# Kernel optimization log

Hardware: AMD Instinct MI355X
Metric: run time of the kernel (lower is better)

Reference implementation:

```python
import jax, jax.numpy as jnp
import numpy as np

H = 768            # hidden_size
IMG_H = 1024       # image_hidden_size
NH = 12            # num_heads
NKV = 1            # num_kv_heads (MQA)
HD = H // NH       # head_dim = 64
FF = 4 * H         # intermediate_size = 3072
EPS = 1e-5


def layernorm(x, g, b):
    m = jnp.mean(x, axis=-1, keepdims=True)
    v = jnp.mean(jnp.square(x - m), axis=-1, keepdims=True)
    return (x - m) * jax.lax.rsqrt(v + EPS) * g + b


def setup_inputs() -> dict:
    key = jax.random.key(0)
    ks = jax.random.split(key, 12)
    B, NQ, NIMG = 8, 256, 4096
    s = 0.02
    return {
        "hidden_states": jax.random.normal(ks[0], (B, NQ, H), jnp.float32),
        "image_features": jax.random.normal(ks[1], (B, NIMG, IMG_H), jnp.float32),
        # norm_image_pre
        "ln_img_g": jnp.ones((IMG_H,), jnp.float32),
        "ln_img_b": jnp.zeros((IMG_H,), jnp.float32),
        # image_bottleneck (bias=False)
        "W_bottle": jax.random.normal(ks[2], (IMG_H, H), jnp.float32) * s,
        # norm_hidden
        "ln_h_g": jnp.ones((H,), jnp.float32),
        "ln_h_b": jnp.zeros((H,), jnp.float32),
        # to_q
        "Wq": jax.random.normal(ks[3], (H, H), jnp.float32) * s,
        "bq": jnp.zeros((H,), jnp.float32),
        # to_kv: out = num_kv_heads * head_dim * 2
        "Wkv": jax.random.normal(ks[4], (H, 2 * NKV * HD), jnp.float32) * s,
        "bkv": jnp.zeros((2 * NKV * HD,), jnp.float32),
        # to_out
        "Wo": jax.random.normal(ks[5], (H, H), jnp.float32) * s,
        "bo": jnp.zeros((H,), jnp.float32),
        # attn_out_norm
        "ln_ao_g": jnp.ones((H,), jnp.float32),
        "ln_ao_b": jnp.zeros((H,), jnp.float32),
        # gate
        "gate_param": jnp.zeros((), jnp.float32),
        # ffn_norm
        "ln_f_g": jnp.ones((H,), jnp.float32),
        "ln_f_b": jnp.zeros((H,), jnp.float32),
        # ffn
        "W1": jax.random.normal(ks[6], (H, FF), jnp.float32) * s,
        "b1": jnp.zeros((FF,), jnp.float32),
        "W2": jax.random.normal(ks[7], (FF, H), jnp.float32) * s,
        "b2": jnp.zeros((H,), jnp.float32),
    }


def reference(hidden_states, image_features, ln_img_g, ln_img_b, W_bottle,
              ln_h_g, ln_h_b, Wq, bq, Wkv, bkv, Wo, bo, ln_ao_g, ln_ao_b,
              gate_param, ln_f_g, ln_f_b, W1, b1, W2, b2):
    B, NQ, _ = hidden_states.shape
    # image pre-norm + bottleneck
    img = layernorm(image_features, ln_img_g, ln_img_b)
    img = img @ W_bottle                                   # [B, Nimg, H]
    # query path
    q_in = layernorm(hidden_states, ln_h_g, ln_h_b)
    q = (q_in @ Wq + bq).reshape(B, NQ, NH, HD).transpose(0, 2, 1, 3)  # b h i d
    # kv path (MQA: single shared KV head)
    kv = (img @ Wkv + bkv).reshape(B, -1, 2, NKV, HD)
    k = kv[:, :, 0, 0, :]                                  # [B, Nimg, HD]
    v = kv[:, :, 1, 0, :]
    scale = 1.0 / np.sqrt(HD)
    # broadcast KV across heads instead of explicit repeat
    scores = jnp.einsum('bhid,bjd->bhij', q * scale, k)    # [B, NH, NQ, Nimg]
    attn = jax.nn.softmax(scores, axis=-1)                 # dropout is identity (eval)
    out = jnp.einsum('bhij,bjd->bhid', attn, v)
    out = out.transpose(0, 2, 1, 3).reshape(B, NQ, H)
    out = out @ Wo + bo
    out = layernorm(out, ln_ao_g, ln_ao_b)
    gate = jax.nn.sigmoid(gate_param)
    h = hidden_states + gate * out
    ffn_in = layernorm(h, ln_f_g, ln_f_b)
    ffn_out = jax.nn.gelu(ffn_in @ W1 + b1, approximate=False) @ W2 + b2
    return h + ffn_out
```

## Files before the change

### kernel.cpp

```cpp
#include <hip/hip_runtime.h>
#include <cstdint>

typedef unsigned short u16;
typedef __bf16 bf16_t;
typedef bf16_t bf16x8 __attribute__((ext_vector_type(8)));
typedef float f32x4 __attribute__((ext_vector_type(4)));

__device__ __forceinline__ float b2f(u16 v) {
  union { uint32_t u; float f; } c; c.u = ((uint32_t)v) << 16; return c.f;
}
__device__ __forceinline__ u16 f2b(float f) {
  union { float f; uint32_t u; } c; c.f = f;
  uint32_t lsb = (c.u >> 16) & 1u;
  return (u16)((c.u + 0x7fffu + lsb) >> 16);
}
__device__ __forceinline__ uint4 pack8(f32x4 a, f32x4 b) {
  union { uint4 v; u16 s[8]; } r;
  r.s[0] = f2b(a[0]); r.s[1] = f2b(a[1]); r.s[2] = f2b(a[2]); r.s[3] = f2b(a[3]);
  r.s[4] = f2b(b[0]); r.s[5] = f2b(b[1]); r.s[6] = f2b(b[2]); r.s[7] = f2b(b[3]);
  return r.v;
}
__device__ __forceinline__ uint32_t cvt_pk_bf16(float lo, float hi) {
  uint32_t r;
  asm("v_cvt_pk_bf16_f32 %0, %1, %2" : "=v"(r) : "v"(lo), "v"(hi));
  return r;
}
__device__ __forceinline__ void phase_barrier() {
  asm volatile("s_waitcnt lgkmcnt(0)" ::: "memory");
  __builtin_amdgcn_s_barrier();
  asm volatile("" ::: "memory");
}
__device__ __forceinline__ void vm_drain() {
  asm volatile("s_waitcnt vmcnt(0)" ::: "memory");
}
template <int N>
__device__ __forceinline__ void vmwait() {
  asm volatile("s_waitcnt vmcnt(%0)" :: "n"(N) : "memory");
}
__device__ __forceinline__ void gload_lds16(const u16* g, u16* l) {
  __builtin_amdgcn_global_load_lds((const __attribute__((address_space(1))) void*)g,
                                   (__attribute__((address_space(3))) void*)l, 16, 0, 0);
}
__device__ __forceinline__ int xcd_swizzle(int lid, int nwg) {
  int q = nwg >> 3, r = nwg & 7, x = lid & 7, s = lid >> 3;
  return (x < r ? x * (q + 1) : r * (q + 1) + (x - r) * q) + s;
}

__global__ __launch_bounds__(256) void prep_main(
    const float* __restrict__ Wq, const float* __restrict__ Wo, const float* __restrict__ W1,
    const float* __restrict__ W2, const float* __restrict__ Wkv,
    u16* __restrict__ WTq, u16* __restrict__ WTo, u16* __restrict__ WT1,
    u16* __restrict__ WT2, u16* __restrict__ WkvT,
    const float* __restrict__ hs, u16* __restrict__ hs16,
    float* __restrict__ rstdq, float* __restrict__ mrstdq,
    const float* __restrict__ img, u16* __restrict__ img16,
    float* __restrict__ rstdi, float* __restrict__ mrstdi) {
  __shared__ __align__(16) u16 tile[32][33];
  int bid = blockIdx.x;
  int lane = threadIdx.x & 63, w = threadIdx.x >> 6;
  if (bid < 5856) {
    const float* in; u16* out; int R, C, gx, tb;
    if (bid < 576)       { in = Wq;  out = WTq;  R = 768;  C = 768;  gx = 24; tb = bid; }
    else if (bid < 1152) { in = Wo;  out = WTo;  R = 768;  C = 768;  gx = 24; tb = bid - 576; }
    else if (bid < 3456) { in = W1;  out = WT1;  R = 768;  C = 3072; gx = 96; tb = bid - 1152; }
    else if (bid < 5760) { in = W2;  out = WT2;  R = 3072; C = 768;  gx = 24; tb = bid - 3456; }
    else                 { in = Wkv; out = WkvT; R = 768;  C = 128;  gx = 4;  tb = bid - 5760; }
    int c0 = (tb % gx) * 32, r0 = (tb / gx) * 32;
    int tx = threadIdx.x & 31, ty = threadIdx.x >> 5;
#pragma unroll
    for (int i = 0; i < 4; ++i) {
      int r = r0 + ty + i * 8, c = c0 + tx;
      tile[ty + i * 8][tx] = f2b(in[(size_t)r * C + c]);
    }
    __syncthreads();
#pragma unroll
    for (int i = 0; i < 4; ++i) {
      int oc = c0 + ty + i * 8, orr = r0 + tx;
      out[(size_t)oc * R + orr] = tile[tx][ty + i * 8];
    }
  } else if (bid < 6368) {
    int row = (bid - 5856) * 4 + w;
    const float* x = hs + (size_t)row * 768;
    float v[12];
#pragma unroll
    for (int it = 0; it < 3; ++it) {
      f32x4 d = *(const f32x4*)(x + (lane + it * 64) * 4);
      v[it * 4 + 0] = d[0]; v[it * 4 + 1] = d[1]; v[it * 4 + 2] = d[2]; v[it * 4 + 3] = d[3];
    }
    float s = 0.f, s2 = 0.f;
#pragma unroll
    for (int i = 0; i < 12; ++i) { s += v[i]; s2 += v[i] * v[i]; }
#pragma unroll
    for (int off = 32; off >= 1; off >>= 1) {
      s += __shfl_xor(s, off, 64);
      s2 += __shfl_xor(s2, off, 64);
    }
    float inv_n = 1.0f / 768.f;
    float mean = s * inv_n;
    float var = fmaxf(s2 * inv_n - mean * mean, 0.f);
    float rstd = rsqrtf(var + 1e-5f);
    if (lane == 0) { rstdq[row] = rstd; mrstdq[row] = mean * rstd; }
#pragma unroll
    for (int it = 0; it < 3; ++it) {
      int c = (lane + it * 64) * 4;
      uint2 po;
      po.x = (uint32_t)f2b(v[it * 4 + 0]) | ((uint32_t)f2b(v[it * 4 + 1]) << 16);
      po.y = (uint32_t)f2b(v[it * 4 + 2]) | ((uint32_t)f2b(v[it * 4 + 3]) << 16);
      *(uint2*)(hs16 + (size_t)row * 768 + c) = po;
    }
  } else {
    int row0 = (bid - 6368) * 16 + w * 4;
    float v[4][16];
#pragma unroll
    for (int r2 = 0; r2 < 4; ++r2) {
      const float* x = img + (size_t)(row0 + r2) * 1024;
#pragma unroll
      for (int it = 0; it < 4; ++it) {
        f32x4 d = *(const f32x4*)(x + (lane + it * 64) * 4);
        v[r2][it * 4 + 0] = d[0]; v[r2][it * 4 + 1] = d[1];
        v[r2][it * 4 + 2] = d[2]; v[r2][it * 4 + 3] = d[3];
      }
    }
#pragma unroll
    for (int r2 = 0; r2 < 4; ++r2) {
      int row = row0 + r2;
      float s = 0.f, s2 = 0.f;
#pragma unroll
      for (int i = 0; i < 16; ++i) { s += v[r2][i]; s2 += v[r2][i] * v[r2][i]; }
#pragma unroll
      for (int off = 32; off >= 1; off >>= 1) {
        s += __shfl_xor(s, off, 64);
        s2 += __shfl_xor(s2, off, 64);
      }
      float inv_n = 1.0f / 1024.f;
      float mean = s * inv_n;
      float var = fmaxf(s2 * inv_n - mean * mean, 0.f);
      float rstd = rsqrtf(var + 1e-5f);
      if (lane == 0) { rstdi[row] = rstd; mrstdi[row] = mean * rstd; }
#pragma unroll
      for (int it = 0; it < 4; ++it) {
        int c = (lane + it * 64) * 4;
        uint2 po;
        po.x = (uint32_t)f2b(v[r2][it * 4 + 0]) | ((uint32_t)f2b(v[r2][it * 4 + 1]) << 16);
        po.y = (uint32_t)f2b(v[r2][it * 4 + 2]) | ((uint32_t)f2b(v[r2][it * 4 + 3]) << 16);
        *(uint2*)(img16 + (size_t)row * 1024 + c) = po;
      }
    }
  }
}

__global__ __launch_bounds__(256) void prep_wg(const u16* __restrict__ WT, const float* __restrict__ g,
                                               const float* __restrict__ b, u16* __restrict__ WgT,
                                               float* __restrict__ ucol, float* __restrict__ wcol,
                                               int K) {
  int n = blockIdx.x * 4 + (threadIdx.x >> 6);
  int lane = threadIdx.x & 63;
  const u16* src = WT + (size_t)n * K;
  u16* dst = WgT + (size_t)n * K;
  float su = 0.f, sw = 0.f;
  for (int k = lane; k < K; k += 64) {
    float wc = b2f(src[k]);
    float wg = g[k] * wc;
    dst[k] = f2b(wg);
    su += wg;
    sw += b[k] * wc;
  }
#pragma unroll
  for (int off = 32; off >= 1; off >>= 1) {
    su += __shfl_xor(su, off, 64);
    sw += __shfl_xor(sw, off, 64);
  }
  if (lane == 0) { ucol[n] = su; wcol[n] = sw; }
}

__global__ __launch_bounds__(256) void ln_res(const u16* __restrict__ ao, const float* __restrict__ g,
                                              const float* __restrict__ bta,
                                              const float* __restrict__ hs,
                                              const float* __restrict__ gatep,
                                              float* __restrict__ hf, u16* __restrict__ hb,
                                              float* __restrict__ rstdg, float* __restrict__ mrstdg) {
  int row = blockIdx.x * 4 + (threadIdx.x >> 6);
  int lane = threadIdx.x & 63;
  const u16* xb = ao + (size_t)row * 768;
  float v[12];
#pragma unroll
  for (int it = 0; it < 3; ++it) {
    int c = (lane + it * 64) * 4;
    uint2 d = *(const uint2*)(xb + c);
    v[it * 4 + 0] = b2f(d.x & 0xffff); v[it * 4 + 1] = b2f(d.x >> 16);
    v[it * 4 + 2] = b2f(d.y & 0xffff); v[it * 4 + 3] = b2f(d.y >> 16);
  }
  float s = 0.f, s2 = 0.f;
#pragma unroll
  for (int i = 0; i < 12; ++i) { s += v[i]; s2 += v[i] * v[i]; }
#pragma unroll
  for (int off = 32; off >= 1; off >>= 1) {
    s += __shfl_xor(s, off, 64);
    s2 += __shfl_xor(s2, off, 64);
  }
  float inv_n = 1.0f / 768.f;
  float mean = s * inv_n;
  float var = fmaxf(s2 * inv_n - mean * mean, 0.f);
  float rstd = rsqrtf(var + 1e-5f);
  float gate = 1.f / (1.f + __expf(-gatep[0]));
  float hsum = 0.f, hsum2 = 0.f;
  float o[12];
#pragma unroll
  for (int it = 0; it < 3; ++it) {
    int c = (lane + it * 64) * 4;
    const float* rr = hs + (size_t)row * 768 + c;
#pragma unroll
    for (int i = 0; i < 4; ++i) {
      float hv = rr[i] + gate * ((v[it * 4 + i] - mean) * rstd * g[c + i] + bta[c + i]);
      o[it * 4 + i] = hv;
      hsum += hv; hsum2 += hv * hv;
    }
    *(f32x4*)(hf + (size_t)row * 768 + c) = (f32x4){o[it * 4 + 0], o[it * 4 + 1], o[it * 4 + 2], o[it * 4 + 3]};
    uint2 po;
    po.x = (uint32_t)f2b(o[it * 4 + 0]) | ((uint32_t)f2b(o[it * 4 + 1]) << 16);
    po.y = (uint32_t)f2b(o[it * 4 + 2]) | ((uint32_t)f2b(o[it * 4 + 3]) << 16);
    *(uint2*)(hb + (size_t)row * 768 + c) = po;
  }
#pragma unroll
  for (int off = 32; off >= 1; off >>= 1) {
    hsum += __shfl_xor(hsum, off, 64);
    hsum2 += __shfl_xor(hsum2, off, 64);
  }
  float hm = hsum * inv_n;
  float hvar = fmaxf(hsum2 * inv_n - hm * hm, 0.f);
  float hrstd = rsqrtf(hvar + 1e-5f);
  if (lane == 0) { rstdg[row] = hrstd; mrstdg[row] = hm * hrstd; }
}

template <int BM, int SPLITK, int AMODE, int BMODE, int EPI, bool OUTF32, bool VTOUT>
__device__ __forceinline__ void gemm_body(u16* __restrict__ aTb, u16* __restrict__ bTb,
                                          const void* __restrict__ Av, const void* __restrict__ Bv,
                                          const float* __restrict__ bias,
                                          const float* __restrict__ rstdg,
                                          const float* __restrict__ mrstdg,
                                          const float* __restrict__ ucol,
                                          const float* __restrict__ wcol,
                                          const float* __restrict__ auxl,
                                          void* __restrict__ Cv, u16* __restrict__ VTout,
                                          int M, int N, int K,
                                          int vgx, int vgy, int vgz, int vlid) {
  constexpr int MT = BM / 32;
  constexpr int AL = BM / 64;
  constexpr bool PURE = (AMODE == 0 && BMODE == 0);
  constexpr int LPT = AL + 2;
  constexpr int ASZ = BM * 32;
  constexpr int BSZ = 128 * 32;

  int nwg = vgx * vgy * vgz;
  int wid = xcd_swizzle(vlid, nwg);
  int bz = wid / (vgx * vgy);
  int rem = wid - bz * (vgx * vgy);
  int bx = rem / vgy;
  int by = rem - bx * vgy;

  int t = threadIdx.x, lane = t & 63, wave = t >> 6;
  int quad = lane >> 4, lcol = lane & 15;
  int wm = (wave >> 1) * (16 * MT), wn = (wave & 1) * 64;
  const u16* Ab = (const u16*)Av;
  const float* Af = (const float*)Av;
  const u16* Bb = (const u16*)Bv;
  const float* Bf = (const float*)Bv;
  const int kchunk = (SPLITK > 1) ? K / SPLITK : K;
  const int kstart = (SPLITK > 1) ? bz * kchunk : 0;
  int rr = t >> 1, rc = t & 1;
  f32x4 acc[MT][4];
#pragma unroll
  for (int i = 0; i < MT; ++i)
#pragma unroll
    for (int j = 0; j < 4; ++j) acc[i][j] = (f32x4){0.f, 0.f, 0.f, 0.f};

  f32x4 braw[4];
  f32x4 am0, am1;

  auto dmaA = [&](int buf, int k0) {
#pragma unroll
    for (int s2 = 0; s2 < AL; ++s2) {
      int row = (wave * AL + s2) * 16 + (lane >> 2);
      int ch = (lane & 3) ^ (row & 3);
      gload_lds16(Ab + (size_t)(bx * BM + row) * K + kstart + k0 + ch * 8,
                  aTb + buf * ASZ + (wave * AL + s2) * 512);
    }
  };
  auto dmaB = [&](int buf, int k0) {
#pragma unroll
    for (int s2 = 0; s2 < 2; ++s2) {
      int row = (wave * 2 + s2) * 16 + (lane >> 2);
      int ch = (lane & 3) ^ (row & 3);
      gload_lds16(Bb + (size_t)(by * 128 + row) * K + kstart + k0 + ch * 8,
                  bTb + buf * BSZ + (wave * 2 + s2) * 512);
    }
  };
  auto loadAmerge = [&](int k0) {
    int c0 = kstart + k0 + (t & 3) * 8;
    int hh = c0 >> 6, dd = c0 & 63;
    int row = bx * 64 + (t >> 2);
    int bb = row >> 8, ii = row & 255;
    am0 = (f32x4){0.f, 0.f, 0.f, 0.f};
    am1 = (f32x4){0.f, 0.f, 0.f, 0.f};
    float lsum = 0.f;
#pragma unroll
    for (int s = 0; s < 4; ++s) {
      size_t base = ((size_t)((bb * 4 + s) * 12 + hh)) * 256 + ii;
      const f32x4* p = (const f32x4*)(Af + base * 64 + dd);
      f32x4 p0 = p[0], p1 = p[1];
#pragma unroll
      for (int j = 0; j < 4; ++j) { am0[j] += p0[j]; am1[j] += p1[j]; }
      lsum += auxl[base];
    }
    float rl = 1.f / lsum;
#pragma unroll
    for (int j = 0; j < 4; ++j) { am0[j] *= rl; am1[j] *= rl; }
  };
  auto storeAmerge = [&](int buf) {
    uint4 c = pack8(am0, am1);
    int ar = t >> 2, ch = t & 3;
    *(uint4*)(aTb + buf * ASZ + ar * 32 + ((ch ^ (ar & 3)) << 3)) = c;
  };
  auto regloadB = [&](int k0) {
    const f32x4* p = (const f32x4*)&Bf[(size_t)(by * 128 + rr) * K + kstart + k0 + rc * 16];
#pragma unroll
    for (int i = 0; i < 4; ++i) braw[i] = p[i];
  };
  auto regstoreB = [&](int buf) {
    uint4 c0 = pack8(braw[0], braw[1]), c1 = pack8(braw[2], braw[3]);
    *(uint4*)(bTb + buf * BSZ + rr * 32 + (((rc * 2 + 0) ^ (rr & 3)) << 3)) = c0;
    *(uint4*)(bTb + buf * BSZ + rr * 32 + (((rc * 2 + 1) ^ (rr & 3)) << 3)) = c1;
  };
  auto compute = [&](int buf) {
    bf16x8 af[MT], bfr[4];
#pragma unroll
    for (int mt = 0; mt < MT; ++mt) {
      int r = wm + mt * 16 + lcol;
      af[mt] = *(const bf16x8*)(aTb + buf * ASZ + r * 32 + (((quad ^ (r & 3))) << 3));
    }
#pragma unroll
    for (int nt = 0; nt < 4; ++nt) {
      int r = wn + nt * 16 + lcol;
      bfr[nt] = *(const bf16x8*)(bTb + buf * BSZ + r * 32 + (((quad ^ (r & 3))) << 3));
    }
#pragma unroll
    for (int mt = 0; mt < MT; ++mt)
#pragma unroll
      for (int nt = 0; nt < 4; ++nt)
        acc[mt][nt] = __builtin_amdgcn_mfma_f32_16x16x32_bf16(af[mt], bfr[nt], acc[mt][nt], 0, 0, 0);
  };

  const int nk = kchunk >> 5;
  if (PURE) {
    dmaA(0, 0); dmaB(0, 0);
    if (nk > 1) { dmaA(1, 1 << 5); dmaB(1, 1 << 5); }
    if (nk > 2) { dmaA(2, 2 << 5); dmaB(2, 2 << 5); }
    for (int kt = 0; kt < nk; ++kt) {
      int left = nk - 1 - kt;
      if (left >= 2) vmwait<2 * LPT>();
      else if (left == 1) vmwait<LPT>();
      else vmwait<0>();
      phase_barrier();
      if (kt + 3 < nk) { dmaA((kt + 3) & 3, (kt + 3) << 5); dmaB((kt + 3) & 3, (kt + 3) << 5); }
      compute(kt & 3);
    }
  } else {
    if (AMODE == 2) loadAmerge(0); else dmaA(0, 0);
    if (BMODE == 1) regloadB(0); else dmaB(0, 0);
    if (AMODE == 2) storeAmerge(0);
    if (BMODE == 1) regstoreB(0);
    vm_drain();
    phase_barrier();
    int cur = 0;
    for (int kt = 0; kt < nk; ++kt) {
      bool more = kt + 1 < nk;
      if (more) {
        if (AMODE == 2) loadAmerge((kt + 1) << 5); else dmaA(cur ^ 1, (kt + 1) << 5);
        if (BMODE == 1) regloadB((kt + 1) << 5); else dmaB(cur ^ 1, (kt + 1) << 5);
      }
      compute(cur);
      if (more) {
        if (AMODE == 2) storeAmerge(cur ^ 1);
        if (BMODE == 1) regstoreB(cur ^ 1);
      }
      vm_drain();
      phase_barrier();
      cur ^= 1;
    }
  }

  if (VTOUT) {
    __syncthreads();
    u16* vtile = aTb;
    u16* kb = (u16*)Cv;
#pragma unroll
    for (int mt = 0; mt < MT; ++mt) {
#pragma unroll
      for (int nt = 0; nt < 4; ++nt) {
#pragma unroll
        for (int r = 0; r < 4; ++r) {
          int lrow = wm + mt * 16 + quad * 4 + r;
          int row = bx * BM + lrow;
          int col = wn + nt * 16 + lcol;
          float v = rstdg[row] * acc[mt][nt][r] - mrstdg[row] * ucol[col] + wcol[col] + bias[col];
          u16 hv = f2b(v);
          if (wn == 0) kb[(size_t)row * 64 + col] = hv;
          else vtile[(col - 64) * 136 + lrow] = hv;
        }
      }
    }
    __syncthreads();
    int dd = t >> 2, js = (t & 3) * 32;
    int bg = bx >> 5, j0g = (bx & 31) * 128;
    u16* dst = VTout + ((size_t)bg * 64 + dd) * 4096 + j0g + js;
#pragma unroll
    for (int i = 0; i < 4; ++i)
      *(uint4*)(dst + i * 8) = *(const uint4*)&vtile[dd * 136 + js + i * 8];
    return;
  }

  u16* Cb = (u16*)Cv;
  float* Cf = (float*)Cv;
  if (SPLITK > 1) Cf += (size_t)bz * (size_t)M * (size_t)N;
#pragma unroll
  for (int mt = 0; mt < MT; ++mt) {
#pragma unroll
    for (int nt = 0; nt < 4; ++nt) {
#pragma unroll
      for (int r = 0; r < 4; ++r) {
        int lrow = wm + mt * 16 + quad * 4 + r;
        int row = bx * BM + lrow;
        int col = by * 128 + wn + nt * 16 + lcol;
        float v = acc[mt][nt][r];
        if (EPI == 1) v += bias[col];
        if (EPI == 3 || EPI == 5)
          v = rstdg[row] * v - mrstdg[row] * ucol[col] + wcol[col] + bias[col];
        if (EPI == 5) v = 0.5f * v * (1.f + erff(v * 0.70710678118f));
        size_t idx = (size_t)row * N + col;
        if (OUTF32) Cf[idx] = v; else Cb[idx] = f2b(v);
      }
    }
  }
}

__global__ __launch_bounds__(256) void prep_fold_wc(
    const u16* __restrict__ WTq, const float* __restrict__ gq, const float* __restrict__ bq_,
    u16* __restrict__ WqgT, float* __restrict__ uq, float* __restrict__ wqv,
    const u16* __restrict__ WT1, const float* __restrict__ g1, const float* __restrict__ b1_,
    u16* __restrict__ W1gT, float* __restrict__ u1, float* __restrict__ w1v,
    const void* __restrict__ WkvT, const void* __restrict__ W_bottle, void* __restrict__ WcT) {
  __shared__ __align__(16) u16 lds[16384];
  int bid = blockIdx.x;
  if (bid < 960) {
    int lane = threadIdx.x & 63, w = threadIdx.x >> 6;
    const u16* WT; const float* g; const float* b; u16* WgT; float* u; float* wv; int n0;
    if (bid < 192) { WT = WTq; g = gq; b = bq_; WgT = WqgT; u = uq; wv = wqv; n0 = bid * 4; }
    else { WT = WT1; g = g1; b = b1_; WgT = W1gT; u = u1; wv = w1v; n0 = (bid - 192) * 4; }
    int n = n0 + w;
    const u16* src = WT + (size_t)n * 768;
    u16* dst = WgT + (size_t)n * 768;
    float su = 0.f, sw = 0.f;
    for (int k = lane; k < 768; k += 64) {
      float wc = b2f(src[k]);
      float wg = g[k] * wc;
      dst[k] = f2b(wg);
      su += wg;
      sw += b[k] * wc;
    }
#pragma unroll
    for (int off = 32; off >= 1; off >>= 1) {
      su += __shfl_xor(su, off, 64);
      sw += __shfl_xor(sw, off, 64);
    }
    if (lane == 0) { u[n] = su; wv[n] = sw; }
  } else {
    gemm_body<128, 1, 0, 1, 0, false, false>(lds, lds + 8192, WkvT, W_bottle, nullptr, nullptr,
                                             nullptr, nullptr, nullptr, nullptr, WcT, nullptr,
                                             128, 1024, 768, 1, 8, 1, bid - 960);
  }
}
__global__ __launch_bounds__(256) void gemm_kvq(
    const void* Akv, const void* Bkv, const float* biaskv, const float* rstdi,
    const float* mrstdi, const float* ui, const float* wi, void* Ckv, u16* VTout,
    const void* Aq, const void* Bq, const float* biasq, const float* rstdq,
    const float* mrstdq, const float* uq, const float* wqv, void* Cq) {
  __shared__ __align__(16) u16 lds[32768];
  int bid = blockIdx.x;
  if (bid < 256) {
    gemm_body<128, 1, 0, 0, 3, false, true>(lds, lds + 16384, Akv, Bkv, biaskv, rstdi, mrstdi,
                                            ui, wi, nullptr, Ckv, VTout,
                                            32768, 128, 1024, 256, 1, 1, bid);
  } else {
    gemm_body<64, 1, 0, 0, 3, false, false>(lds, lds + 8192, Aq, Bq, biasq, rstdq, mrstdq,
                                            uq, wqv, nullptr, Cq, nullptr,
                                            2048, 768, 768, 32, 6, 1, bid - 256);
  }
}
__global__ __launch_bounds__(256) void gemm_o(const void* Av, const void* Bv, const float* bias,
                                              const float* lpart, void* Cv) {
  __shared__ __align__(16) u16 lds[12288];
  int vlid = ((int)blockIdx.y) * 32 + (int)blockIdx.x;
  gemm_body<64, 1, 2, 0, 1, false, false>(lds, lds + 4096, Av, Bv, bias, nullptr, nullptr,
                                          nullptr, nullptr, lpart, Cv, nullptr,
                                          2048, 768, 768, 32, 6, 1, vlid);
}
__global__ __launch_bounds__(256) void gemm_w1(const void* Av, const void* Bv, const float* bias,
                                               const float* rstdg, const float* mrstdg,
                                               const float* ucol, const float* wcol, void* Cv) {
  __shared__ __align__(16) u16 lds[32768];
  int vlid = ((int)blockIdx.y) * 16 + (int)blockIdx.x;
  gemm_body<128, 1, 0, 0, 5, false, false>(lds, lds + 16384, Av, Bv, bias, rstdg, mrstdg,
                                           ucol, wcol, nullptr, Cv, nullptr,
                                           2048, 3072, 768, 16, 24, 1, vlid);
}
__global__ __launch_bounds__(256) void gemm_w2(const void* Av, const void* Bv, void* Cv) {
  __shared__ __align__(16) u16 lds[32768];
  int vlid = (((int)blockIdx.z) * 6 + (int)blockIdx.y) * 16 + (int)blockIdx.x;
  gemm_body<128, 2, 0, 0, 0, true, false>(lds, lds + 16384, Av, Bv, nullptr, nullptr, nullptr,
                                          nullptr, nullptr, nullptr, Cv, nullptr,
                                          2048, 768, 3072, 16, 6, 2, vlid);
}

__global__ __launch_bounds__(256) void w2_merge(const float* __restrict__ part,
                                                const float* __restrict__ hf,
                                                const float* __restrict__ b2,
                                                float* __restrict__ out) {
  int idx = blockIdx.x * 256 + threadIdx.x;
  f32x4 p0 = ((const f32x4*)part)[idx];
  f32x4 p1 = ((const f32x4*)part)[idx + 393216];
  f32x4 h = ((const f32x4*)hf)[idx];
  f32x4 bb = ((const f32x4*)b2)[idx % 192];
  f32x4 o;
#pragma unroll
  for (int i = 0; i < 4; ++i) o[i] = p0[i] + p1[i] + h[i] + bb[i];
  ((f32x4*)out)[idx] = o;
}

__global__ __launch_bounds__(256) void attn_kernel(const u16* __restrict__ qbuf,
                                                   const u16* __restrict__ kb,
                                                   const u16* __restrict__ VT,
                                                   float* __restrict__ Opart,
                                                   float* __restrict__ lpart) {
  __shared__ __align__(16) u16 k_lds[2][64 * 72];
  __shared__ __align__(16) u16 vt_lds[2][64 * 72];
  __shared__ __align__(16) u16 p_lds[4 * 16 * 72];
  int lid = ((int)blockIdx.z * 12 + (int)blockIdx.y) * 4 + (int)blockIdx.x;
  int wid = (lid & 7) * 192 + (lid >> 3);
  int bi = wid & 3;
  int h = (wid >> 2) % 12;
  int z = wid / 48;
  int b = z >> 2, s = z & 3;
  int t = threadIdx.x;
  int wave = t >> 6, lane = t & 63, quad = lane >> 4, lcol = lane & 15;
  int i0 = bi * 64 + wave * 16;
  const u16* qrow = qbuf + ((size_t)(b * 256 + i0 + lcol) * 768 + h * 64 + quad * 8);
  bf16x8 qf0 = *(const bf16x8*)qrow;
  bf16x8 qf1 = *(const bf16x8*)(qrow + 32);
  float l_r[4] = {0.f, 0.f, 0.f, 0.f};
  f32x4 oacc[4];
#pragma unroll
  for (int nt = 0; nt < 4; ++nt) oacc[nt] = (f32x4){0.f, 0.f, 0.f, 0.f};
  int sr = t >> 2, sc = (t & 3) * 16;
  const u16* kbase = kb + (size_t)b * 4096 * 64;
  const u16* vtbase = VT + (size_t)b * 64 * 4096;
  u16* pw = &p_lds[wave * 16 * 72];

  uint4 kr0, kr1, vr0, vr1;
  auto stage_load = [&](int jt) {
    int j0 = s * 1024 + jt * 64;
    const u16* krow = kbase + (size_t)(j0 + sr) * 64 + sc;
    kr0 = *(const uint4*)(krow);
    kr1 = *(const uint4*)(krow + 8);
    const u16* vrow = vtbase + (size_t)sr * 4096 + j0 + sc;
    vr0 = *(const uint4*)(vrow);
    vr1 = *(const uint4*)(vrow + 8);
  };
  auto stage_store = [&](int buf) {
    *(uint4*)&k_lds[buf][sr * 72 + sc] = kr0;
    *(uint4*)&k_lds[buf][sr * 72 + sc + 8] = kr1;
    *(uint4*)&vt_lds[buf][sr * 72 + sc] = vr0;
    *(uint4*)&vt_lds[buf][sr * 72 + sc + 8] = vr1;
  };

  stage_load(0);
  stage_store(0);
  phase_barrier();
  int cur = 0;
  for (int jt = 0; jt < 16; ++jt) {
    bool more = jt + 1 < 16;
    if (more) stage_load(jt + 1);

    f32x4 sc4[4];
#pragma unroll
    for (int nt = 0; nt < 4; ++nt) sc4[nt] = (f32x4){0.f, 0.f, 0.f, 0.f};
    __builtin_amdgcn_s_setprio(1);
#pragma unroll
    for (int nt = 0; nt < 4; ++nt) {
      bf16x8 kb0 = *(const bf16x8*)&k_lds[cur][(nt * 16 + lcol) * 72 + quad * 8];
      bf16x8 kb1 = *(const bf16x8*)&k_lds[cur][(nt * 16 + lcol) * 72 + 32 + quad * 8];
      sc4[nt] = __builtin_amdgcn_mfma_f32_16x16x32_bf16(qf0, kb0, sc4[nt], 0, 0, 0);
      sc4[nt] = __builtin_amdgcn_mfma_f32_16x16x32_bf16(qf1, kb1, sc4[nt], 0, 0, 0);
    }
    __builtin_amdgcn_s_setprio(0);
#pragma unroll
    for (int r = 0; r < 4; ++r) {
      float rsum = 0.f;
#pragma unroll
      for (int nt = 0; nt < 4; ++nt) {
        float p = __expf(sc4[nt][r] * 0.125f);
        sc4[nt][r] = p;
        rsum += p;
      }
      rsum += __shfl_xor(rsum, 1, 64);
      rsum += __shfl_xor(rsum, 2, 64);
      rsum += __shfl_xor(rsum, 4, 64);
      rsum += __shfl_xor(rsum, 8, 64);
      l_r[r] += rsum;
      uint32_t pk01 = cvt_pk_bf16(sc4[0][r], sc4[1][r]);
      uint32_t pk23 = cvt_pk_bf16(sc4[2][r], sc4[3][r]);
      int prow = (quad * 4 + r) * 72 + lcol;
      pw[prow] = (u16)(pk01 & 0xffff);
      pw[prow + 16] = (u16)(pk01 >> 16);
      pw[prow + 32] = (u16)(pk23 & 0xffff);
      pw[prow + 48] = (u16)(pk23 >> 16);
    }
    __builtin_amdgcn_s_setprio(1);
#pragma unroll
    for (int ks = 0; ks < 2; ++ks) {
      bf16x8 pa = *(const bf16x8*)&pw[lcol * 72 + ks * 32 + quad * 8];
#pragma unroll
      for (int nt = 0; nt < 4; ++nt) {
        bf16x8 vb = *(const bf16x8*)&vt_lds[cur][(nt * 16 + lcol) * 72 + ks * 32 + quad * 8];
        oacc[nt] = __builtin_amdgcn_mfma_f32_16x16x32_bf16(pa, vb, oacc[nt], 0, 0, 0);
      }
    }
    __builtin_amdgcn_s_setprio(0);
    if (more) stage_store(cur ^ 1);
    phase_barrier();
    cur ^= 1;
  }
  size_t base = ((size_t)z * 12 + h) * 256;
#pragma unroll
  for (int r = 0; r < 4; ++r) {
    int row = bi * 64 + wave * 16 + quad * 4 + r;
#pragma unroll
    for (int nt = 0; nt < 4; ++nt)
      Opart[(base + row) * 64 + nt * 16 + lcol] = oacc[nt][r];
    if (lcol == 0) lpart[base + row] = l_r[r];
  }
}

extern "C" void kernel_launch(void* const* d_in, const int* in_sizes, int n_in, void* d_out,
                              int out_size, void* d_ws, size_t ws_size, hipStream_t stream) {
  (void)in_sizes; (void)n_in; (void)out_size; (void)ws_size;
  const float* hs = (const float*)d_in[0];
  const float* imgf = (const float*)d_in[1];
  const float* ln_img_g = (const float*)d_in[2];
  const float* ln_img_b = (const float*)d_in[3];
  const float* W_bottle = (const float*)d_in[4];
  const float* ln_h_g = (const float*)d_in[5];
  const float* ln_h_b = (const float*)d_in[6];
  const float* Wq = (const float*)d_in[7];
  const float* bq = (const float*)d_in[8];
  const float* Wkv = (const float*)d_in[9];
  const float* bkv = (const float*)d_in[10];
  const float* Wo = (const float*)d_in[11];
  const float* bo = (const float*)d_in[12];
  const float* ln_ao_g = (const float*)d_in[13];
  const float* ln_ao_b = (const float*)d_in[14];
  const float* gatep = (const float*)d_in[15];
  const float* ln_f_g = (const float*)d_in[16];
  const float* ln_f_b = (const float*)d_in[17];
  const float* W1 = (const float*)d_in[18];
  const float* b1 = (const float*)d_in[19];
  const float* W2 = (const float*)d_in[20];
  const float* b2 = (const float*)d_in[21];

  char* sc = (char*)d_ws;
  auto alloc = [&](size_t bytes) {
    char* p = sc;
    sc += (bytes + 63) & ~(size_t)63;
    return p;
  };
  u16* WTq = (u16*)alloc(768 * 768 * 2);
  u16* WTo = (u16*)alloc(768 * 768 * 2);
  u16* WT1 = (u16*)alloc(3072 * 768 * 2);
  u16* WT2 = (u16*)alloc(768 * 3072 * 2);
  u16* WkvT = (u16*)alloc(128 * 768 * 2);
  u16* WcT = (u16*)alloc(128 * 1024 * 2);
  u16* WgT = (u16*)alloc(128 * 1024 * 2);
  u16* WqgT = (u16*)alloc(768 * 768 * 2);
  u16* W1gT = (u16*)alloc(3072 * 768 * 2);
  float* ucol = (float*)alloc(128 * 4);
  float* wcol = (float*)alloc(128 * 4);
  float* uq = (float*)alloc(768 * 4);
  float* wq = (float*)alloc(768 * 4);
  float* u1 = (float*)alloc(3072 * 4);
  float* w1c = (float*)alloc(3072 * 4);
  float* rstdq = (float*)alloc(2048 * 4);
  float* mrstdq = (float*)alloc(2048 * 4);
  float* rstdh = (float*)alloc(2048 * 4);
  float* mrstdh = (float*)alloc(2048 * 4);
  float* rstdi = (float*)alloc(32768 * 4);
  float* mrstdi = (float*)alloc(32768 * 4);
  u16* hs16 = (u16*)alloc(2048 * 768 * 2);
  u16* img16 = (u16*)alloc((size_t)32768 * 1024 * 2);
  u16* kb = (u16*)alloc((size_t)32768 * 64 * 2);
  u16* VT = (u16*)alloc((size_t)8 * 64 * 4096 * 2);
  u16* qb = (u16*)alloc(2048 * 768 * 2);
  u16* ao = (u16*)alloc(2048 * 768 * 2);
  u16* hbuf = (u16*)alloc(2048 * 768 * 2);
  float* hf32 = (float*)alloc(2048 * 768 * 4);
  u16* actb = (u16*)alloc((size_t)2048 * 3072 * 2);
  float* Opart = (float*)alloc((size_t)32 * 12 * 256 * 64 * 4);
  float* lpart = (float*)alloc((size_t)32 * 12 * 256 * 4);

  prep_main<<<8416, 256, 0, stream>>>(Wq, Wo, W1, W2, Wkv, WTq, WTo, WT1, WT2, WkvT,
                                      hs, hs16, rstdq, mrstdq,
                                      imgf, img16, rstdi, mrstdi);
  prep_fold_wc<<<968, 256, 0, stream>>>(WTq, ln_h_g, ln_h_b, WqgT, uq, wq,
                                        WT1, ln_f_g, ln_f_b, W1gT, u1, w1c,
                                        WkvT, W_bottle, WcT);
  prep_wg<<<32, 256, 0, stream>>>(WcT, ln_img_g, ln_img_b, WgT, ucol, wcol, 1024);
  gemm_kvq<<<448, 256, 0, stream>>>(img16, WgT, bkv, rstdi, mrstdi, ucol, wcol, kb, VT,
                                    hs16, WqgT, bq, rstdq, mrstdq, uq, wq, qb);
  attn_kernel<<<dim3(4, 12, 32), 256, 0, stream>>>(qb, kb, VT, Opart, lpart);
  gemm_o<<<dim3(32, 6), 256, 0, stream>>>(Opart, WTo, bo, lpart, ao);
  ln_res<<<512, 256, 0, stream>>>(ao, ln_ao_g, ln_ao_b, hs, gatep, hf32, hbuf, rstdh, mrstdh);
  gemm_w1<<<dim3(16, 24), 256, 0, stream>>>(hbuf, W1gT, b1, rstdh, mrstdh, u1, w1c, actb);
  gemm_w2<<<dim3(16, 6, 2), 256, 0, stream>>>(actb, WT2, Opart);
  w2_merge<<<1536, 256, 0, stream>>>(Opart, hf32, b2, (float*)d_out);
}
```

Before: 494.4 us.

## Fuse image layernorm stats and bf16 conversion into KV GEMM A-load

Removes the separate image-feature pass in prep_main that converted the 32768x1024 fp32 image features to bf16 and computed per-row mean/rstd. The KV GEMM now loads fp32 image rows directly into registers, converts them to bf16 into LDS, and accumulates sum and sum of squares along K. Row statistics are reduced at the end into shared memory and used in the epilogue. This avoids writing and rereading a 64MB bf16 intermediate, at the cost of register-path loads instead of direct-to-LDS DMA and heavier per-thread work in the KV GEMM.

```diff
diff --git a/kernel.cpp b/kernel.cpp
--- a/kernel.cpp
+++ b/kernel.cpp
@@ -52,9 +52,7 @@
     u16* __restrict__ WTq, u16* __restrict__ WTo, u16* __restrict__ WT1,
     u16* __restrict__ WT2, u16* __restrict__ WkvT,
     const float* __restrict__ hs, u16* __restrict__ hs16,
-    float* __restrict__ rstdq, float* __restrict__ mrstdq,
-    const float* __restrict__ img, u16* __restrict__ img16,
-    float* __restrict__ rstdi, float* __restrict__ mrstdi) {
+    float* __restrict__ rstdq, float* __restrict__ mrstdq) {
   __shared__ __align__(16) u16 tile[32][33];
   int bid = blockIdx.x;
   int lane = threadIdx.x & 63, w = threadIdx.x >> 6;
@@ -78,7 +76,7 @@
       int oc = c0 + ty + i * 8, orr = r0 + tx;
       out[(size_t)oc * R + orr] = tile[tx][ty + i * 8];
     }
-  } else if (bid < 6368) {
+  } else {
     int row = (bid - 5856) * 4 + w;
     const float* x = hs + (size_t)row * 768;
     float v[12];
@@ -107,44 +105,6 @@
       po.x = (uint32_t)f2b(v[it * 4 + 0]) | ((uint32_t)f2b(v[it * 4 + 1]) << 16);
       po.y = (uint32_t)f2b(v[it * 4 + 2]) | ((uint32_t)f2b(v[it * 4 + 3]) << 16);
       *(uint2*)(hs16 + (size_t)row * 768 + c) = po;
-    }
-  } else {
-    int row0 = (bid - 6368) * 16 + w * 4;
-    float v[4][16];
-#pragma unroll
-    for (int r2 = 0; r2 < 4; ++r2) {
-      const float* x = img + (size_t)(row0 + r2) * 1024;
-#pragma unroll
-      for (int it = 0; it < 4; ++it) {
-        f32x4 d = *(const f32x4*)(x + (lane + it * 64) * 4);
-        v[r2][it * 4 + 0] = d[0]; v[r2][it * 4 + 1] = d[1];
-        v[r2][it * 4 + 2] = d[2]; v[r2][it * 4 + 3] = d[3];
-      }
-    }
-#pragma unroll
-    for (int r2 = 0; r2 < 4; ++r2) {
-      int row = row0 + r2;
-      float s = 0.f, s2 = 0.f;
-#pragma unroll
-      for (int i = 0; i < 16; ++i) { s += v[r2][i]; s2 += v[r2][i] * v[r2][i]; }
-#pragma unroll
-      for (int off = 32; off >= 1; off >>= 1) {
-        s += __shfl_xor(s, off, 64);
-        s2 += __shfl_xor(s2, off, 64);
-      }
-      float inv_n = 1.0f / 1024.f;
-      float mean = s * inv_n;
-      float var = fmaxf(s2 * inv_n - mean * mean, 0.f);
-      float rstd = rsqrtf(var + 1e-5f);
-      if (lane == 0) { rstdi[row] = rstd; mrstdi[row] = mean * rstd; }
-#pragma unroll
-      for (int it = 0; it < 4; ++it) {
-        int c = (lane + it * 64) * 4;
-        uint2 po;
-        po.x = (uint32_t)f2b(v[r2][it * 4 + 0]) | ((uint32_t)f2b(v[r2][it * 4 + 1]) << 16);
-        po.y = (uint32_t)f2b(v[r2][it * 4 + 2]) | ((uint32_t)f2b(v[r2][it * 4 + 3]) << 16);
-        *(uint2*)(img16 + (size_t)row * 1024 + c) = po;
-      }
     }
   }
 }
@@ -250,6 +210,8 @@
   constexpr int LPT = AL + 2;
   constexpr int ASZ = BM * 32;
   constexpr int BSZ = 128 * 32;
+  __shared__ float rstd_s[EPI == 4 ? 128 : 1];
+  __shared__ float mrstd_s[EPI == 4 ? 128 : 1];
 
   int nwg = vgx * vgy * vgz;
   int wid = xcd_swizzle(vlid, nwg);
@@ -268,13 +230,14 @@
   const int kchunk = (SPLITK > 1) ? K / SPLITK : K;
   const int kstart = (SPLITK > 1) ? bz * kchunk : 0;
   int rr = t >> 1, rc = t & 1;
+  float sa = 0.f, sa2 = 0.f;
   f32x4 acc[MT][4];
 #pragma unroll
   for (int i = 0; i < MT; ++i)
 #pragma unroll
     for (int j = 0; j < 4; ++j) acc[i][j] = (f32x4){0.f, 0.f, 0.f, 0.f};
 
-  f32x4 braw[4];
+  f32x4 araw[4], braw[4];
   f32x4 am0, am1;
 
   auto dmaA = [&](int buf, int k0) {
@@ -294,6 +257,22 @@
       gload_lds16(Bb + (size_t)(by * 128 + row) * K + kstart + k0 + ch * 8,
                   bTb + buf * BSZ + (wave * 2 + s2) * 512);
     }
+  };
+  auto regloadA = [&](int k0) {
+    const f32x4* p = (const f32x4*)&Af[(size_t)(bx * BM + rr) * K + kstart + k0 + rc * 16];
+#pragma unroll
+    for (int i = 0; i < 4; ++i) araw[i] = p[i];
+  };
+  auto regstoreA = [&](int buf) {
+    if (EPI == 4) {
+#pragma unroll
+      for (int i = 0; i < 4; ++i)
+#pragma unroll
+        for (int j = 0; j < 4; ++j) { sa += araw[i][j]; sa2 += araw[i][j] * araw[i][j]; }
+    }
+    uint4 c0 = pack8(araw[0], araw[1]), c1 = pack8(araw[2], araw[3]);
+    *(uint4*)(aTb + buf * ASZ + rr * 32 + (((rc * 2 + 0) ^ (rr & 3)) << 3)) = c0;
+    *(uint4*)(aTb + buf * ASZ + rr * 32 + (((rc * 2 + 1) ^ (rr & 3)) << 3)) = c1;
   };
   auto loadAmerge = [&](int k0) {
     int c0 = kstart + k0 + (t & 3) * 8;
@@ -365,8 +344,9 @@
       compute(kt & 3);
     }
   } else {
-    if (AMODE == 2) loadAmerge(0); else dmaA(0, 0);
+    if (AMODE == 1) regloadA(0); else if (AMODE == 2) loadAmerge(0); else dmaA(0, 0);
     if (BMODE == 1) regloadB(0); else dmaB(0, 0);
+    if (AMODE == 1) regstoreA(0);
     if (AMODE == 2) storeAmerge(0);
     if (BMODE == 1) regstoreB(0);
     vm_drain();
@@ -375,11 +355,14 @@
     for (int kt = 0; kt < nk; ++kt) {
       bool more = kt + 1 < nk;
       if (more) {
-        if (AMODE == 2) loadAmerge((kt + 1) << 5); else dmaA(cur ^ 1, (kt + 1) << 5);
+        if (AMODE == 1) regloadA((kt + 1) << 5);
+        else if (AMODE == 2) loadAmerge((kt + 1) << 5);
+        else dmaA(cur ^ 1, (kt + 1) << 5);
         if (BMODE == 1) regloadB((kt + 1) << 5); else dmaB(cur ^ 1, (kt + 1) << 5);
       }
       compute(cur);
       if (more) {
+        if (AMODE == 1) regstoreA(cur ^ 1);
         if (AMODE == 2) storeAmerge(cur ^ 1);
         if (BMODE == 1) regstoreB(cur ^ 1);
       }
@@ -389,6 +372,21 @@
     }
   }
 
+  if (EPI == 4) {
+    float s = sa, s2 = sa2;
+    s += __shfl_xor(s, 1, 64);
+    s2 += __shfl_xor(s2, 1, 64);
+    if ((t & 1) == 0) {
+      float inv_n = 1.0f / (float)K;
+      float mean = s * inv_n;
+      float var = fmaxf(s2 * inv_n - mean * mean, 0.f);
+      float rstd = rsqrtf(var + 1e-5f);
+      rstd_s[rr] = rstd;
+      mrstd_s[rr] = mean * rstd;
+    }
+    __syncthreads();
+  }
+
   if (VTOUT) {
     __syncthreads();
     u16* vtile = aTb;
@@ -402,7 +400,9 @@
           int lrow = wm + mt * 16 + quad * 4 + r;
           int row = bx * BM + lrow;
           int col = wn + nt * 16 + lcol;
-          float v = rstdg[row] * acc[mt][nt][r] - mrstdg[row] * ucol[col] + wcol[col] + bias[col];
+          float R = (EPI == 4) ? rstd_s[lrow] : rstdg[row];
+          float MR = (EPI == 4) ? mrstd_s[lrow] : mrstdg[row];
+          float v = R * acc[mt][nt][r] - MR * ucol[col] + wcol[col] + bias[col];
           u16 hv = f2b(v);
           if (wn == 0) kb[(size_t)row * 64 + col] = hv;
           else vtile[(col - 64) * 136 + lrow] = hv;
@@ -435,6 +435,8 @@
         if (EPI == 1) v += bias[col];
         if (EPI == 3 || EPI == 5)
           v = rstdg[row] * v - mrstdg[row] * ucol[col] + wcol[col] + bias[col];
+        if (EPI == 4)
+          v = rstd_s[lrow] * v - mrstd_s[lrow] * ucol[col] + wcol[col] + bias[col];
         if (EPI == 5) v = 0.5f * v * (1.f + erff(v * 0.70710678118f));
         size_t idx = (size_t)row * N + col;
         if (OUTF32) Cf[idx] = v; else Cb[idx] = f2b(v);
@@ -480,14 +482,14 @@
   }
 }
 __global__ __launch_bounds__(256) void gemm_kvq(
-    const void* Akv, const void* Bkv, const float* biaskv, const float* rstdi,
-    const float* mrstdi, const float* ui, const float* wi, void* Ckv, u16* VTout,
+    const void* Akv, const void* Bkv, const float* biaskv,
+    const float* ui, const float* wi, void* Ckv, u16* VTout,
     const void* Aq, const void* Bq, const float* biasq, const float* rstdq,
     const float* mrstdq, const float* uq, const float* wqv, void* Cq) {
   __shared__ __align__(16) u16 lds[32768];
   int bid = blockIdx.x;
   if (bid < 256) {
-    gemm_body<128, 1, 0, 0, 3, false, true>(lds, lds + 16384, Akv, Bkv, biaskv, rstdi, mrstdi,
+    gemm_body<128, 1, 1, 0, 4, false, true>(lds, lds + 8192, Akv, Bkv, biaskv, nullptr, nullptr,
                                             ui, wi, nullptr, Ckv, VTout,
                                             32768, 128, 1024, 256, 1, 1, bid);
   } else {
@@ -701,10 +703,7 @@
   float* mrstdq = (float*)alloc(2048 * 4);
   float* rstdh = (float*)alloc(2048 * 4);
   float* mrstdh = (float*)alloc(2048 * 4);
-  float* rstdi = (float*)alloc(32768 * 4);
-  float* mrstdi = (float*)alloc(32768 * 4);
   u16* hs16 = (u16*)alloc(2048 * 768 * 2);
-  u16* img16 = (u16*)alloc((size_t)32768 * 1024 * 2);
   u16* kb = (u16*)alloc((size_t)32768 * 64 * 2);
   u16* VT = (u16*)alloc((size_t)8 * 64 * 4096 * 2);
   u16* qb = (u16*)alloc(2048 * 768 * 2);
@@ -715,14 +714,13 @@
   float* Opart = (float*)alloc((size_t)32 * 12 * 256 * 64 * 4);
   float* lpart = (float*)alloc((size_t)32 * 12 * 256 * 4);
 
-  prep_main<<<8416, 256, 0, stream>>>(Wq, Wo, W1, W2, Wkv, WTq, WTo, WT1, WT2, WkvT,
-                                      hs, hs16, rstdq, mrstdq,
-                                      imgf, img16, rstdi, mrstdi);
+  prep_main<<<6368, 256, 0, stream>>>(Wq, Wo, W1, W2, Wkv, WTq, WTo, WT1, WT2, WkvT,
+                                      hs, hs16, rstdq, mrstdq);
   prep_fold_wc<<<968, 256, 0, stream>>>(WTq, ln_h_g, ln_h_b, WqgT, uq, wq,
                                         WT1, ln_f_g, ln_f_b, W1gT, u1, w1c,
                                         WkvT, W_bottle, WcT);
   prep_wg<<<32, 256, 0, stream>>>(WcT, ln_img_g, ln_img_b, WgT, ucol, wcol, 1024);
-  gemm_kvq<<<448, 256, 0, stream>>>(img16, WgT, bkv, rstdi, mrstdi, ucol, wcol, kb, VT,
+  gemm_kvq<<<448, 256, 0, stream>>>(imgf, WgT, bkv, ucol, wcol, kb, VT,
                                     hs16, WqgT, bq, rstdq, mrstdq, uq, wq, qb);
   attn_kernel<<<dim3(4, 12, 32), 256, 0, stream>>>(qb, kb, VT, Opart, lpart);
   gemm_o<<<dim3(32, 6), 256, 0, stream>>>(Opart, WTo, bo, lpart, ao);
```

New measurement: 483.0 us. 2.3% less time.
